# Kernel optimization log

Hardware: AMD Instinct MI355X
Metric: run time of the kernel (lower is better)

Reference implementation:

```python
import jax, jax.numpy as jnp
import numpy as np
from jax import lax

H = 1024       # hidden_size
I = 1024       # intermediate_size (per expert)
E = 16         # num_experts
TOP_K = 4      # num_active_experts


def setup_inputs() -> dict:
    key = jax.random.key(0)
    ks = jax.random.split(key, 9)
    std_gate = 0.02 / (E ** 0.5)
    return {
        "hidden_states": jax.random.normal(ks[0], (1, 2048, H), jnp.float32),
        "gate_w": jax.random.normal(ks[1], (E, H), jnp.float32) * std_gate,
        "expert_bias": jnp.zeros((E,), jnp.float32),
        "w1": jax.random.normal(ks[2], (E, I, H), jnp.float32) * 0.02,
        "w2": jax.random.normal(ks[3], (E, H, I), jnp.float32) * 0.02,
        "w3": jax.random.normal(ks[4], (E, I, H), jnp.float32) * 0.02,
        "sw1": jax.random.normal(ks[5], (I, H), jnp.float32) * 0.02,
        "sw2": jax.random.normal(ks[6], (H, I), jnp.float32) * 0.02,
        "sw3": jax.random.normal(ks[7], (I, H), jnp.float32) * 0.02,
    }


def _swiglu(x, wg, wd, wu):
    # Swish(x W1^T) * (x W3^T) then W2^T
    return (jax.nn.silu(x @ wg.T) * (x @ wu.T)) @ wd.T


def reference(hidden_states, gate_w, expert_bias, w1, w2, w3, sw1, sw2, sw3):
    B, S, Hd = hidden_states.shape
    x = hidden_states.reshape(-1, Hd)              # [T, H]
    T = x.shape[0]

    # ---- Router ----
    router_logits = x @ gate_w.T                   # [T, E]
    biased = router_logits + expert_bias           # loss-free balancing bias
    _, sel = lax.top_k(biased, TOP_K)              # [T, K] indices from biased logits
    raw = jnp.take_along_axis(router_logits, sel, axis=-1)  # weights from UNbiased logits
    rw = jax.nn.softmax(raw.astype(jnp.float32), axis=-1).astype(x.dtype)  # [T, K]

    # Dense combine weights g[t, e] = routing weight if e selected else 0
    g = jnp.zeros((T, E), x.dtype).at[jnp.arange(T)[:, None], sel].add(rw)

    # ---- Routed experts (mathematically equal to grouped dispatch) ----
    routed = jnp.zeros_like(x)
    for e in range(E):  # fixed small expert loop
        routed = routed + g[:, e:e + 1] * _swiglu(x, w1[e], w2[e], w3[e])

    # ---- Shared expert ----
    shared = _swiglu(x, sw1, sw2, sw3)

    out = (shared + routed).reshape(B, S, Hd)      # dropout p=0 -> identity
    return out
```

## Files before the change

kernel.cpp:

```cpp
#include <hip/hip_runtime.h>
#include <cstddef>
#include <cstdint>

#define T_TOK 2048
#define HD 1024
#define ID 1024
#define NE 16
#define TOPK 4
#define BM 128
#define BN 128
#define BK 32
#define MT_MAX 96
#define SLOT_CAP (MT_MAX * BM)

typedef float f32x4 __attribute__((ext_vector_type(4)));
typedef __bf16 bf16x8 __attribute__((ext_vector_type(8)));
typedef __bf16 bf16x4 __attribute__((ext_vector_type(4)));

#define WS_TILE_E 256
#define WS_LOGITS (256 + 8192 * 4 * 2 + 1024)
#define WS_SLOT_TOK (WS_LOGITS + T_TOK * NE * 4)
#define WS_SLOT_W (WS_SLOT_TOK + SLOT_CAP * 4)
#define WS_H1 (WS_SLOT_W + SLOT_CAP * 4)
#define WS_XB (WS_H1 + (size_t)SLOT_CAP * ID * 2)
#define WS_W1B (WS_XB + (size_t)T_TOK * HD * 2)
#define WS_W2B (WS_W1B + (size_t)NE * ID * HD * 2)
#define WS_W3B (WS_W2B + (size_t)NE * HD * ID * 2)
#define WS_SW1B (WS_W3B + (size_t)NE * ID * HD * 2)
#define WS_SW2B (WS_SW1B + (size_t)ID * HD * 2)
#define WS_SW3B (WS_SW2B + (size_t)HD * ID * 2)
#define WS_NEED (WS_SW3B + (size_t)ID * HD * 2)

__device__ __forceinline__ f32x4 mfma16(bf16x8 a, bf16x8 b, f32x4 c) {
  return __builtin_amdgcn_mfma_f32_16x16x32_bf16(a, b, c, 0, 0, 0);
}

__device__ __forceinline__ void st_bf16x4(__bf16* dst, float4 v) {
  __bf16 tmp[4] = {(__bf16)v.x, (__bf16)v.y, (__bf16)v.z, (__bf16)v.w};
  *(uint2*)dst = *(const uint2*)tmp;
}

__device__ __forceinline__ void gload16(const __bf16* g, __bf16* l) {
  __builtin_amdgcn_global_load_lds(
      (const __attribute__((address_space(1))) uint32_t*)g,
      (__attribute__((address_space(3))) uint32_t*)l, 16, 0, 0);
}

#define W4 ((size_t)1 << 22)
#define S4 ((size_t)1 << 18)
#define X4 ((size_t)1 << 19)
#define CVT4_TOTAL (3 * W4 + 3 * S4 + X4)
#define CVT_GRID 2048
#define LOGITS_BLOCKS (T_TOK / 4)

__global__ __launch_bounds__(256) void fused_pre(
    const float* __restrict__ w1, const float* __restrict__ w2,
    const float* __restrict__ w3, const float* __restrict__ sw1,
    const float* __restrict__ sw2, const float* __restrict__ sw3,
    const float* __restrict__ x, __bf16* __restrict__ w1b,
    __bf16* __restrict__ w2b, __bf16* __restrict__ w3b,
    __bf16* __restrict__ sw1b, __bf16* __restrict__ sw2b,
    __bf16* __restrict__ sw3b, __bf16* __restrict__ xb,
    const float* __restrict__ gw, float* __restrict__ logits) {
  int tid = threadIdx.x;
  if ((int)blockIdx.x < LOGITS_BLOCKS) {
    int wv = tid >> 6;
    int lane = tid & 63;
    int tok = blockIdx.x * 4 + wv;
    int e = lane >> 2;
    int q = lane & 3;
    const float4* xr = (const float4*)(x + (size_t)tok * HD) + q * 64;
    const float4* wr = (const float4*)(gw + (size_t)e * HD) + q * 64;
    float s0 = 0.f, s1 = 0.f;
#pragma unroll 8
    for (int i = 0; i < 64; i += 2) {
      float4 a0 = xr[i], w0 = wr[i];
      float4 a1 = xr[i + 1], w1v = wr[i + 1];
      s0 += a0.x * w0.x + a0.y * w0.y + a0.z * w0.z + a0.w * w0.w;
      s1 += a1.x * w1v.x + a1.y * w1v.y + a1.z * w1v.z + a1.w * w1v.w;
    }
    float s = s0 + s1;
    s += __shfl_xor(s, 1);
    s += __shfl_xor(s, 2);
    if (q == 0) logits[(size_t)tok * NE + e] = s;
    return;
  }
  size_t b = blockIdx.x - LOGITS_BLOCKS;
  const size_t stride = (size_t)CVT_GRID * 256;
  for (size_t i = b * 256 + tid; i < CVT4_TOTAL; i += stride) {
    const float* src;
    __bf16* dst;
    size_t off;
    if (i < 3 * W4) {
      size_t t = i >> 22;
      off = i & (W4 - 1);
      src = (t == 0) ? w1 : (t == 1) ? w2 : w3;
      dst = (t == 0) ? w1b : (t == 1) ? w2b : w3b;
    } else {
      size_t j = i - 3 * W4;
      if (j < 3 * S4) {
        size_t t = j >> 18;
        off = j & (S4 - 1);
        src = (t == 0) ? sw1 : (t == 1) ? sw2 : sw3;
        dst = (t == 0) ? sw1b : (t == 1) ? sw2b : sw3b;
      } else {
        off = j - 3 * S4;
        src = x;
        dst = xb;
      }
    }
    f32x4 v = __builtin_nontemporal_load((const f32x4*)src + off);
    bf16x4 o = {(__bf16)v[0], (__bf16)v[1], (__bf16)v[2], (__bf16)v[3]};
    *(bf16x4*)(dst + 4 * off) = o;
  }
}

__global__ __launch_bounds__(256) void router_logits(
    const float* __restrict__ x, const float* __restrict__ gw,
    float* __restrict__ logits) {
  int tid = threadIdx.x;
  int wv = tid >> 6;
  int lane = tid & 63;
  int tok = blockIdx.x * 4 + wv;
  int e = lane >> 2;
  int q = lane & 3;
  const float4* xr = (const float4*)(x + (size_t)tok * HD) + q * 64;
  const float4* wr = (const float4*)(gw + (size_t)e * HD) + q * 64;
  float s0 = 0.f, s1 = 0.f;
#pragma unroll 8
  for (int i = 0; i < 64; i += 2) {
    float4 a0 = xr[i], w0 = wr[i];
    float4 a1 = xr[i + 1], w1 = wr[i + 1];
    s0 += a0.x * w0.x + a0.y * w0.y + a0.z * w0.z + a0.w * w0.w;
    s1 += a1.x * w1.x + a1.y * w1.y + a1.z * w1.z + a1.w * w1.w;
  }
  float s = s0 + s1;
  s += __shfl_xor(s, 1);
  s += __shfl_xor(s, 2);
  if (q == 0) logits[(size_t)tok * NE + e] = s;
}

__global__ __launch_bounds__(256) void router_finish(
    const float* __restrict__ logits, const float* __restrict__ bias,
    int* __restrict__ tile_e, int* __restrict__ slot_tok,
    float* __restrict__ slot_w) {
  __shared__ int hist[NE];
  __shared__ int soff[NE + 1];
  __shared__ int fillp[NE];
  __shared__ unsigned lsel[T_TOK];
  __shared__ float4 lw4[T_TOK];

  int tid = threadIdx.x;
  if (tid < NE) { hist[tid] = 0; fillp[tid] = 0; }
  __syncthreads();

  float bb[NE];
#pragma unroll
  for (int e = 0; e < NE; ++e) bb[e] = bias[e];

  for (int j = 0; j < T_TOK / 256; ++j) {
    int t = tid + 256 * j;
    float lg[NE];
    const float4* lp = (const float4*)(logits + (size_t)t * NE);
#pragma unroll
    for (int q = 0; q < 4; ++q) {
      float4 v = lp[q];
      lg[4 * q] = v.x; lg[4 * q + 1] = v.y; lg[4 * q + 2] = v.z; lg[4 * q + 3] = v.w;
    }
    float b[NE];
#pragma unroll
    for (int e = 0; e < NE; ++e) b[e] = lg[e] + bb[e];

    int selk[TOPK];
    float raw[TOPK];
    unsigned used = 0;
#pragma unroll
    for (int k = 0; k < TOPK; ++k) {
      float best = -3.4e38f;
      int bi = 0;
#pragma unroll
      for (int e = 0; e < NE; ++e) {
        if (!((used >> e) & 1) && b[e] > best) { best = b[e]; bi = e; }
      }
      used |= (1u << bi);
      selk[k] = bi;
      raw[k] = lg[bi];
    }
    float m = raw[0];
#pragma unroll
    for (int k = 1; k < TOPK; ++k) m = fmaxf(m, raw[k]);
    float s = 0.f;
    float w[TOPK];
#pragma unroll
    for (int k = 0; k < TOPK; ++k) { w[k] = __expf(raw[k] - m); s += w[k]; }
    float inv = 1.f / s;
    lsel[t] = (unsigned)selk[0] | ((unsigned)selk[1] << 8) |
              ((unsigned)selk[2] << 16) | ((unsigned)selk[3] << 24);
    lw4[t] = make_float4(w[0] * inv, w[1] * inv, w[2] * inv, w[3] * inv);
#pragma unroll
    for (int k = 0; k < TOPK; ++k) atomicAdd(&hist[selk[k]], 1);
  }
  __syncthreads();

  if (tid == 0) {
    int o = 0;
    for (int e = 0; e < NE; ++e) { soff[e] = o; o += (hist[e] + BM - 1) & ~(BM - 1); }
    soff[NE] = o;
  }
  __syncthreads();
  int shared_base = soff[NE];
  int total = shared_base + T_TOK;
  for (int tt = tid; tt < MT_MAX; tt += 256) {
    int base = tt * BM;
    int ee = -1;
    if (base < shared_base) {
      ee = 0;
#pragma unroll
      for (int q = 1; q < NE; ++q) if (base >= soff[q]) ee = q;
    } else if (base < total) {
      ee = NE;
    }
    tile_e[tt] = ee;
  }

  for (int j = 0; j < T_TOK / 256; ++j) {
    int t = tid + 256 * j;
    unsigned ps = lsel[t];
    float4 wv = lw4[t];
    int e0 = ps & 255, e1 = (ps >> 8) & 255, e2 = (ps >> 16) & 255, e3 = ps >> 24;
    int p0 = atomicAdd(&fillp[e0], 1);
    slot_tok[soff[e0] + p0] = t; slot_w[soff[e0] + p0] = wv.x;
    int p1 = atomicAdd(&fillp[e1], 1);
    slot_tok[soff[e1] + p1] = t; slot_w[soff[e1] + p1] = wv.y;
    int p2 = atomicAdd(&fillp[e2], 1);
    slot_tok[soff[e2] + p2] = t; slot_w[soff[e2] + p2] = wv.z;
    int p3 = atomicAdd(&fillp[e3], 1);
    slot_tok[soff[e3] + p3] = t; slot_w[soff[e3] + p3] = wv.w;
  }

  for (int s = tid; s < shared_base; s += 256) {
    int e = 0;
#pragma unroll
    for (int q = 1; q < NE; ++q) if (s >= soff[q]) e = q;
    if (s >= soff[e] + hist[e]) { slot_tok[s] = -1; slot_w[s] = 0.f; }
  }
  for (int s = shared_base + tid; s < total; s += 256) {
    slot_tok[s] = s - shared_base;
    slot_w[s] = 1.0f;
  }
}


__global__ __launch_bounds__(256, 2) void pass1_bf16(
    const __bf16* __restrict__ xb, const int* __restrict__ slot_tok,
    const int* __restrict__ tile_e, const __bf16* __restrict__ w1b,
    const __bf16* __restrict__ w3b, const __bf16* __restrict__ sw1b,
    const __bf16* __restrict__ sw3b, __bf16* __restrict__ h1) {
  int mt = blockIdx.y;
  int e = tile_e[mt];
  if (e < 0) return;
  int n0 = blockIdx.x * BN;
  int m0 = mt * BM;

  const __bf16* wg = (e == NE) ? sw1b : w1b + (size_t)e * ID * HD;
  const __bf16* wu = (e == NE) ? sw3b : w3b + (size_t)e * ID * HD;

  __shared__ __align__(16) __bf16 As[2][BM * BK];
  __shared__ __align__(16) __bf16 Bg[2][BN * BK];
  __shared__ __align__(16) __bf16 Bu[2][BN * BK];

  int tid = threadIdx.x;
  int r0 = tid >> 2, r1 = r0 + 64;
  int c8 = ((tid & 3) ^ ((r0 >> 1) & 3)) * 8;
  int tok0 = slot_tok[m0 + r0]; if (tok0 < 0) tok0 = 0;
  int tok1 = slot_tok[m0 + r1]; if (tok1 < 0) tok1 = 0;
  const __bf16* gA0 = xb + (size_t)tok0 * HD + c8;
  const __bf16* gA1 = xb + (size_t)tok1 * HD + c8;
  const __bf16* gG0 = wg + (size_t)(n0 + r0) * HD + c8;
  const __bf16* gG1 = wg + (size_t)(n0 + r1) * HD + c8;
  const __bf16* gU0 = wu + (size_t)(n0 + r0) * HD + c8;
  const __bf16* gU1 = wu + (size_t)(n0 + r1) * HD + c8;

  int wave = tid >> 6, lane = tid & 63;
  int wm = (wave >> 1) * 64, wn = (wave & 1) * 64;
  int l16 = lane & 15, kch = lane >> 4;
  int kk8 = (kch ^ ((l16 >> 1) & 3)) * 8;

  f32x4 accg[4][4] = {};
  f32x4 accu[4][4] = {};

  auto stage = [&](int B, int k0) {
    gload16(gA0 + k0, &As[B][(size_t)tid * 8]);
    gload16(gA1 + k0, &As[B][(size_t)(tid + 256) * 8]);
    gload16(gG0 + k0, &Bg[B][(size_t)tid * 8]);
    gload16(gG1 + k0, &Bg[B][(size_t)(tid + 256) * 8]);
    gload16(gU0 + k0, &Bu[B][(size_t)tid * 8]);
    gload16(gU1 + k0, &Bu[B][(size_t)(tid + 256) * 8]);
  };
  auto body = [&](int B) {
    bf16x8 af[4], gf[4], uf[4];
#pragma unroll
    for (int i = 0; i < 4; ++i) {
      af[i] = *(const bf16x8*)(&As[B][(wm + i * 16 + l16) * BK + kk8]);
      gf[i] = *(const bf16x8*)(&Bg[B][(wn + i * 16 + l16) * BK + kk8]);
      uf[i] = *(const bf16x8*)(&Bu[B][(wn + i * 16 + l16) * BK + kk8]);
    }
    asm volatile("s_waitcnt lgkmcnt(0)" ::: "memory");
    __builtin_amdgcn_s_barrier();
    __builtin_amdgcn_sched_barrier(0);
#pragma unroll
    for (int mi = 0; mi < 4; ++mi)
#pragma unroll
      for (int ni = 0; ni < 4; ++ni) {
        accg[mi][ni] = mfma16(af[mi], gf[ni], accg[mi][ni]);
        accu[mi][ni] = mfma16(af[mi], uf[ni], accu[mi][ni]);
      }
  };

  stage(0, 0);
#pragma unroll 1
  for (int k = 0; k < HD / BK - 1; ++k) {
    int cur = k & 1;
    stage(cur ^ 1, (k + 1) * BK);
    asm volatile("s_waitcnt vmcnt(6)" ::: "memory");
    __builtin_amdgcn_s_barrier();
    __builtin_amdgcn_sched_barrier(0);
    body(cur);
  }
  asm volatile("s_waitcnt vmcnt(0)" ::: "memory");
  __builtin_amdgcn_s_barrier();
  __builtin_amdgcn_sched_barrier(0);
  body((HD / BK - 1) & 1);

#pragma unroll
  for (int mi = 0; mi < 4; ++mi) {
#pragma unroll
    for (int ni = 0; ni < 4; ++ni) {
#pragma unroll
      for (int j = 0; j < 4; ++j) {
        int row = m0 + wm + mi * 16 + kch * 4 + j;
        int col = n0 + wn + ni * 16 + l16;
        float g = accg[mi][ni][j];
        float u = accu[mi][ni][j];
        float hv = (g / (1.f + __expf(-g))) * u;
        h1[(size_t)row * ID + col] = (__bf16)hv;
      }
    }
  }
}

__global__ __launch_bounds__(256, 3) void pass2_bf16(
    const __bf16* __restrict__ h1, const int* __restrict__ slot_tok,
    const float* __restrict__ slot_w, const int* __restrict__ tile_e,
    const __bf16* __restrict__ w2b, const __bf16* __restrict__ sw2b,
    float* __restrict__ out) {
  int mt = blockIdx.y;
  int e = tile_e[mt];
  if (e < 0) return;
  int n0 = blockIdx.x * BN;
  int m0 = mt * BM;

  const __bf16* wd = (e == NE) ? sw2b : w2b + (size_t)e * HD * ID;

  __shared__ __align__(16) __bf16 As[2][BM * BK];
  __shared__ __align__(16) __bf16 Bs[2][BN * BK];

  int tid = threadIdx.x;
  int r0 = tid >> 2, r1 = r0 + 64;
  int c8 = ((tid & 3) ^ ((r0 >> 1) & 3)) * 8;
  const __bf16* gA0 = h1 + (size_t)(m0 + r0) * ID + c8;
  const __bf16* gA1 = h1 + (size_t)(m0 + r1) * ID + c8;
  const __bf16* gB0 = wd + (size_t)(n0 + r0) * ID + c8;
  const __bf16* gB1 = wd + (size_t)(n0 + r1) * ID + c8;

  int wave = tid >> 6, lane = tid & 63;
  int wm = (wave >> 1) * 64, wn = (wave & 1) * 64;
  int l16 = lane & 15, kch = lane >> 4;
  int kk8 = (kch ^ ((l16 >> 1) & 3)) * 8;

  f32x4 acc[4][4] = {};

  auto stage = [&](int B, int k0) {
    gload16(gA0 + k0, &As[B][(size_t)tid * 8]);
    gload16(gA1 + k0, &As[B][(size_t)(tid + 256) * 8]);
    gload16(gB0 + k0, &Bs[B][(size_t)tid * 8]);
    gload16(gB1 + k0, &Bs[B][(size_t)(tid + 256) * 8]);
  };
  auto body = [&](int B) {
    bf16x8 af[4], bf[4];
#pragma unroll
    for (int i = 0; i < 4; ++i) {
      af[i] = *(const bf16x8*)(&As[B][(wm + i * 16 + l16) * BK + kk8]);
      bf[i] = *(const bf16x8*)(&Bs[B][(wn + i * 16 + l16) * BK + kk8]);
    }
    asm volatile("s_waitcnt lgkmcnt(0)" ::: "memory");
    __builtin_amdgcn_s_barrier();
    __builtin_amdgcn_sched_barrier(0);
#pragma unroll
    for (int mi = 0; mi < 4; ++mi)
#pragma unroll
      for (int ni = 0; ni < 4; ++ni)
        acc[mi][ni] = mfma16(af[mi], bf[ni], acc[mi][ni]);
  };

  stage(0, 0);
#pragma unroll 1
  for (int k = 0; k < ID / BK - 1; ++k) {
    int cur = k & 1;
    stage(cur ^ 1, (k + 1) * BK);
    asm volatile("s_waitcnt vmcnt(4)" ::: "memory");
    __builtin_amdgcn_s_barrier();
    __builtin_amdgcn_sched_barrier(0);
    body(cur);
  }
  asm volatile("s_waitcnt vmcnt(0)" ::: "memory");
  __builtin_amdgcn_s_barrier();
  __builtin_amdgcn_sched_barrier(0);
  body((ID / BK - 1) & 1);

#pragma unroll
  for (int mi = 0; mi < 4; ++mi) {
#pragma unroll
    for (int j = 0; j < 4; ++j) {
      int row = m0 + wm + mi * 16 + kch * 4 + j;
      int token = slot_tok[row];
      if (token < 0) continue;
      float wgt = slot_w[row];
#pragma unroll
      for (int ni = 0; ni < 4; ++ni) {
        int col = n0 + wn + ni * 16 + l16;
        atomicAdd(out + (size_t)token * HD + col, wgt * acc[mi][ni][j]);
      }
    }
  }
}


__global__ __launch_bounds__(256, 2) void pass1_gemm(
    const float* __restrict__ x, const int* __restrict__ slot_tok,
    const int* __restrict__ tile_e, const float* __restrict__ w1,
    const float* __restrict__ w3, const float* __restrict__ sw1,
    const float* __restrict__ sw3, __bf16* __restrict__ h1) {
  int mt = blockIdx.x;
  int e = tile_e[mt];
  if (e < 0) return;
  int n0 = blockIdx.y * BN;
  int m0 = mt * BM;

  const float* wg;
  const float* wu;
  if (e == NE) { wg = sw1; wu = sw3; }
  else { wg = w1 + (size_t)e * ID * HD; wu = w3 + (size_t)e * ID * HD; }

  __shared__ __bf16 As[BM][BK + 8];
  __shared__ __bf16 Bg[BN][BK + 8];
  __shared__ __bf16 Bu[BN][BK + 8];

  int tid = threadIdx.x;
  int lrow = tid >> 1;
  int lcol = (tid & 1) * 16;
  int tokenA = slot_tok[m0 + lrow];
  const float* aptr = x + (size_t)(tokenA < 0 ? 0 : tokenA) * HD + lcol;
  const float* gptr = wg + (size_t)(n0 + lrow) * HD + lcol;
  const float* uptr = wu + (size_t)(n0 + lrow) * HD + lcol;

  int wave = tid >> 6, lane = tid & 63;
  int wm = (wave >> 1) * 64, wn = (wave & 1) * 64;
  int l16 = lane & 15, kch = lane >> 4;

  f32x4 accg[4][4] = {};
  f32x4 accu[4][4] = {};

  for (int k0 = 0; k0 < HD; k0 += BK) {
    float4 av[4], gv[4], uv[4];
#pragma unroll
    for (int j = 0; j < 4; ++j) {
      av[j] = (tokenA >= 0) ? *(const float4*)(aptr + k0 + 4 * j)
                            : make_float4(0.f, 0.f, 0.f, 0.f);
      gv[j] = *(const float4*)(gptr + k0 + 4 * j);
      uv[j] = *(const float4*)(uptr + k0 + 4 * j);
    }
    __syncthreads();
#pragma unroll
    for (int j = 0; j < 4; ++j) {
      st_bf16x4(&As[lrow][lcol + 4 * j], av[j]);
      st_bf16x4(&Bg[lrow][lcol + 4 * j], gv[j]);
      st_bf16x4(&Bu[lrow][lcol + 4 * j], uv[j]);
    }
    __syncthreads();

    bf16x8 af[4], gf[4], uf[4];
#pragma unroll
    for (int i = 0; i < 4; ++i) {
      af[i] = *(const bf16x8*)(&As[wm + i * 16 + l16][kch * 8]);
      gf[i] = *(const bf16x8*)(&Bg[wn + i * 16 + l16][kch * 8]);
      uf[i] = *(const bf16x8*)(&Bu[wn + i * 16 + l16][kch * 8]);
    }
#pragma unroll
    for (int mi = 0; mi < 4; ++mi)
#pragma unroll
      for (int ni = 0; ni < 4; ++ni) {
        accg[mi][ni] = mfma16(af[mi], gf[ni], accg[mi][ni]);
        accu[mi][ni] = mfma16(af[mi], uf[ni], accu[mi][ni]);
      }
  }

#pragma unroll
  for (int mi = 0; mi < 4; ++mi) {
#pragma unroll
    for (int ni = 0; ni < 4; ++ni) {
#pragma unroll
      for (int j = 0; j < 4; ++j) {
        int row = m0 + wm + mi * 16 + kch * 4 + j;
        int col = n0 + wn + ni * 16 + l16;
        float g = accg[mi][ni][j];
        float u = accu[mi][ni][j];
        float hv = (g / (1.f + __expf(-g))) * u;
        h1[(size_t)row * ID + col] = (__bf16)hv;
      }
    }
  }
}

__global__ __launch_bounds__(256, 2) void pass2_gemm(
    const __bf16* __restrict__ h1, const int* __restrict__ slot_tok,
    const float* __restrict__ slot_w, const int* __restrict__ tile_e,
    const float* __restrict__ w2, const float* __restrict__ sw2,
    float* __restrict__ out) {
  int mt = blockIdx.x;
  int e = tile_e[mt];
  if (e < 0) return;
  int n0 = blockIdx.y * BN;
  int m0 = mt * BM;

  const float* wd = (e == NE) ? sw2 : (w2 + (size_t)e * HD * ID);

  __shared__ __bf16 As[BM][BK + 8];
  __shared__ __bf16 Bs[BN][BK + 8];

  int tid = threadIdx.x;
  int lrow = tid >> 1;
  int lcol = (tid & 1) * 16;
  const __bf16* aptr = h1 + (size_t)(m0 + lrow) * ID + lcol;
  const float* bptr = wd + (size_t)(n0 + lrow) * ID + lcol;

  int wave = tid >> 6, lane = tid & 63;
  int wm = (wave >> 1) * 64, wn = (wave & 1) * 64;
  int l16 = lane & 15, kch = lane >> 4;

  f32x4 acc[4][4] = {};

  for (int k0 = 0; k0 < ID; k0 += BK) {
    uint4 a0 = *(const uint4*)(aptr + k0);
    uint4 a1 = *(const uint4*)(aptr + k0 + 8);
    float4 bv[4];
#pragma unroll
    for (int j = 0; j < 4; ++j) bv[j] = *(const float4*)(bptr + k0 + 4 * j);
    __syncthreads();
    *(uint4*)(&As[lrow][lcol]) = a0;
    *(uint4*)(&As[lrow][lcol + 8]) = a1;
#pragma unroll
    for (int j = 0; j < 4; ++j) st_bf16x4(&Bs[lrow][lcol + 4 * j], bv[j]);
    __syncthreads();

    bf16x8 af[4], bf[4];
#pragma unroll
    for (int i = 0; i < 4; ++i) {
      af[i] = *(const bf16x8*)(&As[wm + i * 16 + l16][kch * 8]);
      bf[i] = *(const bf16x8*)(&Bs[wn + i * 16 + l16][kch * 8]);
    }
#pragma unroll
    for (int mi = 0; mi < 4; ++mi)
#pragma unroll
      for (int ni = 0; ni < 4; ++ni)
        acc[mi][ni] = mfma16(af[mi], bf[ni], acc[mi][ni]);
  }

#pragma unroll
  for (int mi = 0; mi < 4; ++mi) {
#pragma unroll
    for (int j = 0; j < 4; ++j) {
      int row = m0 + wm + mi * 16 + kch * 4 + j;
      int token = slot_tok[row];
      if (token < 0) continue;
      float wgt = slot_w[row];
#pragma unroll
      for (int ni = 0; ni < 4; ++ni) {
        int col = n0 + wn + ni * 16 + l16;
        atomicAdd(out + (size_t)token * HD + col, wgt * acc[mi][ni][j]);
      }
    }
  }
}

extern "C" void kernel_launch(void* const* d_in, const int* in_sizes, int n_in,
                              void* d_out, int out_size, void* d_ws, size_t ws_size,
                              hipStream_t stream) {
  const float* x = (const float*)d_in[0];
  const float* gate_w = (const float*)d_in[1];
  const float* ebias = (const float*)d_in[2];
  const float* w1 = (const float*)d_in[3];
  const float* w2 = (const float*)d_in[4];
  const float* w3 = (const float*)d_in[5];
  const float* sw1 = (const float*)d_in[6];
  const float* sw2 = (const float*)d_in[7];
  const float* sw3 = (const float*)d_in[8];
  float* out = (float*)d_out;

  char* ws = (char*)d_ws;
  int* tile_e = (int*)(ws + WS_TILE_E);
  float* logits = (float*)(ws + WS_LOGITS);
  int* slot_tok = (int*)(ws + WS_SLOT_TOK);
  float* slot_w = (float*)(ws + WS_SLOT_W);
  __bf16* h1 = (__bf16*)(ws + WS_H1);

  hipMemsetAsync(d_out, 0, (size_t)T_TOK * HD * sizeof(float), stream);

  if (ws_size >= WS_NEED) {
    __bf16* xb = (__bf16*)(ws + WS_XB);
    __bf16* w1b = (__bf16*)(ws + WS_W1B);
    __bf16* w2b = (__bf16*)(ws + WS_W2B);
    __bf16* w3b = (__bf16*)(ws + WS_W3B);
    __bf16* sw1b = (__bf16*)(ws + WS_SW1B);
    __bf16* sw2b = (__bf16*)(ws + WS_SW2B);
    __bf16* sw3b = (__bf16*)(ws + WS_SW3B);

    fused_pre<<<LOGITS_BLOCKS + CVT_GRID, 256, 0, stream>>>(
        w1, w2, w3, sw1, sw2, sw3, x, w1b, w2b, w3b, sw1b, sw2b, sw3b, xb,
        gate_w, logits);
    router_finish<<<1, 256, 0, stream>>>(logits, ebias, tile_e, slot_tok, slot_w);

    pass1_bf16<<<dim3(ID / BN, MT_MAX), 256, 0, stream>>>(
        xb, slot_tok, tile_e, w1b, w3b, sw1b, sw3b, h1);
    pass2_bf16<<<dim3(HD / BN, MT_MAX), 256, 0, stream>>>(
        h1, slot_tok, slot_w, tile_e, w2b, sw2b, out);
  } else {
    router_logits<<<T_TOK / 4, 256, 0, stream>>>(x, gate_w, logits);
    router_finish<<<1, 256, 0, stream>>>(logits, ebias, tile_e, slot_tok, slot_w);
    pass1_gemm<<<dim3(MT_MAX, ID / BN), 256, 0, stream>>>(x, slot_tok, tile_e, w1,
                                                          w3, sw1, sw3, h1);
    pass2_gemm<<<dim3(MT_MAX, HD / BN), 256, 0, stream>>>(h1, slot_tok, slot_w,
                                                          tile_e, w2, sw2, out);
  }
}
```

Baseline: 256.6 us.

## Convert w1/w3 to bf16 inside pass1 instead of a separate pre-pass

The pre-pass no longer converts the w1, w3, sw1 and sw3 weights to bf16. It now converts only w2, sw2 and x, using 8-wide vector stores. pass1 reads the fp32 gate and up weights directly, converts them in registers and writes them into double-buffered swizzled LDS. The activation tile still arrives through direct global-to-LDS loads. This drops one full fp32 read plus bf16 write and reread of about 64 MB of weights. The cost is that each weight tile is reread in fp32 once per m-tile, and pass1 now waits on vmcnt(0) synchronously. The fallback fp32 kernels and the workspace size check are removed.

```diff
diff --git a/kernel.cpp b/kernel.cpp
--- a/kernel.cpp
+++ b/kernel.cpp
@@ -10,34 +10,32 @@
 #define BM 128
 #define BN 128
 #define BK 32
+#define NK1 (HD / BK)
 #define MT_MAX 96
 #define SLOT_CAP (MT_MAX * BM)
 
 typedef float f32x4 __attribute__((ext_vector_type(4)));
 typedef __bf16 bf16x8 __attribute__((ext_vector_type(8)));
-typedef __bf16 bf16x4 __attribute__((ext_vector_type(4)));
 
 #define WS_TILE_E 256
-#define WS_LOGITS (256 + 8192 * 4 * 2 + 1024)
+#define WS_LOGITS 4096
 #define WS_SLOT_TOK (WS_LOGITS + T_TOK * NE * 4)
 #define WS_SLOT_W (WS_SLOT_TOK + SLOT_CAP * 4)
 #define WS_H1 (WS_SLOT_W + SLOT_CAP * 4)
 #define WS_XB (WS_H1 + (size_t)SLOT_CAP * ID * 2)
-#define WS_W1B (WS_XB + (size_t)T_TOK * HD * 2)
-#define WS_W2B (WS_W1B + (size_t)NE * ID * HD * 2)
-#define WS_W3B (WS_W2B + (size_t)NE * HD * ID * 2)
-#define WS_SW1B (WS_W3B + (size_t)NE * ID * HD * 2)
-#define WS_SW2B (WS_SW1B + (size_t)ID * HD * 2)
-#define WS_SW3B (WS_SW2B + (size_t)HD * ID * 2)
-#define WS_NEED (WS_SW3B + (size_t)ID * HD * 2)
+#define WS_W2B (WS_XB + (size_t)T_TOK * HD * 2)
+#define WS_SW2B (WS_W2B + (size_t)NE * HD * ID * 2)
+#define WS_NEED (WS_SW2B + (size_t)ID * HD * 2)
 
 __device__ __forceinline__ f32x4 mfma16(bf16x8 a, bf16x8 b, f32x4 c) {
   return __builtin_amdgcn_mfma_f32_16x16x32_bf16(a, b, c, 0, 0, 0);
 }
 
-__device__ __forceinline__ void st_bf16x4(__bf16* dst, float4 v) {
-  __bf16 tmp[4] = {(__bf16)v.x, (__bf16)v.y, (__bf16)v.z, (__bf16)v.w};
-  *(uint2*)dst = *(const uint2*)tmp;
+__device__ __forceinline__ bf16x8 pack8(float4 a, float4 b) {
+  bf16x8 o;
+  o[0] = (__bf16)a.x; o[1] = (__bf16)a.y; o[2] = (__bf16)a.z; o[3] = (__bf16)a.w;
+  o[4] = (__bf16)b.x; o[5] = (__bf16)b.y; o[6] = (__bf16)b.z; o[7] = (__bf16)b.w;
+  return o;
 }
 
 __device__ __forceinline__ void gload16(const __bf16* g, __bf16* l) {
@@ -46,21 +44,17 @@
       (__attribute__((address_space(3))) uint32_t*)l, 16, 0, 0);
 }
 
-#define W4 ((size_t)1 << 22)
-#define S4 ((size_t)1 << 18)
-#define X4 ((size_t)1 << 19)
-#define CVT4_TOTAL (3 * W4 + 3 * S4 + X4)
-#define CVT_GRID 2048
+#define W2G ((size_t)NE * HD * ID / 8)
+#define SWG ((size_t)ID * HD / 8)
+#define XG ((size_t)T_TOK * HD / 8)
+#define CVT_TOT (W2G + SWG + XG)
+#define CVTB 1536
 #define LOGITS_BLOCKS (T_TOK / 4)
 
 __global__ __launch_bounds__(256) void fused_pre(
-    const float* __restrict__ w1, const float* __restrict__ w2,
-    const float* __restrict__ w3, const float* __restrict__ sw1,
-    const float* __restrict__ sw2, const float* __restrict__ sw3,
-    const float* __restrict__ x, __bf16* __restrict__ w1b,
-    __bf16* __restrict__ w2b, __bf16* __restrict__ w3b,
-    __bf16* __restrict__ sw1b, __bf16* __restrict__ sw2b,
-    __bf16* __restrict__ sw3b, __bf16* __restrict__ xb,
+    const float* __restrict__ w2, const float* __restrict__ sw2,
+    const float* __restrict__ x, __bf16* __restrict__ w2b,
+    __bf16* __restrict__ sw2b, __bf16* __restrict__ xb,
     const float* __restrict__ gw, float* __restrict__ logits) {
   int tid = threadIdx.x;
   if ((int)blockIdx.x < LOGITS_BLOCKS) {
@@ -86,58 +80,18 @@
     return;
   }
   size_t b = blockIdx.x - LOGITS_BLOCKS;
-  const size_t stride = (size_t)CVT_GRID * 256;
-  for (size_t i = b * 256 + tid; i < CVT4_TOTAL; i += stride) {
+  const size_t stride = (size_t)CVTB * 256;
+  for (size_t i = b * 256 + tid; i < CVT_TOT; i += stride) {
     const float* src;
     __bf16* dst;
     size_t off;
-    if (i < 3 * W4) {
-      size_t t = i >> 22;
-      off = i & (W4 - 1);
-      src = (t == 0) ? w1 : (t == 1) ? w2 : w3;
-      dst = (t == 0) ? w1b : (t == 1) ? w2b : w3b;
-    } else {
-      size_t j = i - 3 * W4;
-      if (j < 3 * S4) {
-        size_t t = j >> 18;
-        off = j & (S4 - 1);
-        src = (t == 0) ? sw1 : (t == 1) ? sw2 : sw3;
-        dst = (t == 0) ? sw1b : (t == 1) ? sw2b : sw3b;
-      } else {
-        off = j - 3 * S4;
-        src = x;
-        dst = xb;
-      }
-    }
-    f32x4 v = __builtin_nontemporal_load((const f32x4*)src + off);
-    bf16x4 o = {(__bf16)v[0], (__bf16)v[1], (__bf16)v[2], (__bf16)v[3]};
-    *(bf16x4*)(dst + 4 * off) = o;
-  }
-}
-
-__global__ __launch_bounds__(256) void router_logits(
-    const float* __restrict__ x, const float* __restrict__ gw,
-    float* __restrict__ logits) {
-  int tid = threadIdx.x;
-  int wv = tid >> 6;
-  int lane = tid & 63;
-  int tok = blockIdx.x * 4 + wv;
-  int e = lane >> 2;
-  int q = lane & 3;
-  const float4* xr = (const float4*)(x + (size_t)tok * HD) + q * 64;
-  const float4* wr = (const float4*)(gw + (size_t)e * HD) + q * 64;
-  float s0 = 0.f, s1 = 0.f;
-#pragma unroll 8
-  for (int i = 0; i < 64; i += 2) {
-    float4 a0 = xr[i], w0 = wr[i];
-    float4 a1 = xr[i + 1], w1 = wr[i + 1];
-    s0 += a0.x * w0.x + a0.y * w0.y + a0.z * w0.z + a0.w * w0.w;
-    s1 += a1.x * w1.x + a1.y * w1.y + a1.z * w1.z + a1.w * w1.w;
-  }
-  float s = s0 + s1;
-  s += __shfl_xor(s, 1);
-  s += __shfl_xor(s, 2);
-  if (q == 0) logits[(size_t)tok * NE + e] = s;
+    if (i < W2G) { src = w2; dst = w2b; off = i; }
+    else if (i < W2G + SWG) { src = sw2; dst = sw2b; off = i - W2G; }
+    else { src = x; dst = xb; off = i - W2G - SWG; }
+    const float4* p = (const float4*)src + 2 * off;
+    float4 a = p[0], c = p[1];
+    *(bf16x8*)(dst + 8 * off) = pack8(a, c);
+  }
 }
 
 __global__ __launch_bounds__(256) void router_finish(
@@ -250,20 +204,19 @@
   }
 }
 
-
 __global__ __launch_bounds__(256, 2) void pass1_bf16(
     const __bf16* __restrict__ xb, const int* __restrict__ slot_tok,
-    const int* __restrict__ tile_e, const __bf16* __restrict__ w1b,
-    const __bf16* __restrict__ w3b, const __bf16* __restrict__ sw1b,
-    const __bf16* __restrict__ sw3b, __bf16* __restrict__ h1) {
+    const int* __restrict__ tile_e, const float* __restrict__ w1,
+    const float* __restrict__ w3, const float* __restrict__ sw1,
+    const float* __restrict__ sw3, __bf16* __restrict__ h1) {
   int mt = blockIdx.y;
   int e = tile_e[mt];
   if (e < 0) return;
   int n0 = blockIdx.x * BN;
   int m0 = mt * BM;
 
-  const __bf16* wg = (e == NE) ? sw1b : w1b + (size_t)e * ID * HD;
-  const __bf16* wu = (e == NE) ? sw3b : w3b + (size_t)e * ID * HD;
+  const float* wg = (e == NE) ? sw1 : w1 + (size_t)e * ID * HD;
+  const float* wu = (e == NE) ? sw3 : w3 + (size_t)e * ID * HD;
 
   __shared__ __align__(16) __bf16 As[2][BM * BK];
   __shared__ __align__(16) __bf16 Bg[2][BN * BK];
@@ -276,10 +229,14 @@
   int tok1 = slot_tok[m0 + r1]; if (tok1 < 0) tok1 = 0;
   const __bf16* gA0 = xb + (size_t)tok0 * HD + c8;
   const __bf16* gA1 = xb + (size_t)tok1 * HD + c8;
-  const __bf16* gG0 = wg + (size_t)(n0 + r0) * HD + c8;
-  const __bf16* gG1 = wg + (size_t)(n0 + r1) * HD + c8;
-  const __bf16* gU0 = wu + (size_t)(n0 + r0) * HD + c8;
-  const __bf16* gU1 = wu + (size_t)(n0 + r1) * HD + c8;
+
+  int brow = tid >> 1;
+  int bhalf = tid & 1;
+  int bsw = (brow >> 1) & 3;
+  const float* gW = wg + (size_t)(n0 + brow) * HD + bhalf * 16;
+  const float* gU = wu + (size_t)(n0 + brow) * HD + bhalf * 16;
+  int slot0 = (((bhalf * 2) ^ bsw) * 8) + brow * BK;
+  int slot1 = (((bhalf * 2 + 1) ^ bsw) * 8) + brow * BK;
 
   int wave = tid >> 6, lane = tid & 63;
   int wm = (wave >> 1) * 64, wn = (wave & 1) * 64;
@@ -289,24 +246,53 @@
   f32x4 accg[4][4] = {};
   f32x4 accu[4][4] = {};
 
-  auto stage = [&](int B, int k0) {
-    gload16(gA0 + k0, &As[B][(size_t)tid * 8]);
-    gload16(gA1 + k0, &As[B][(size_t)(tid + 256) * 8]);
-    gload16(gG0 + k0, &Bg[B][(size_t)tid * 8]);
-    gload16(gG1 + k0, &Bg[B][(size_t)(tid + 256) * 8]);
-    gload16(gU0 + k0, &Bu[B][(size_t)tid * 8]);
-    gload16(gU1 + k0, &Bu[B][(size_t)(tid + 256) * 8]);
-  };
-  auto body = [&](int B) {
-    bf16x8 af[4], gf[4], uf[4];
-#pragma unroll
-    for (int i = 0; i < 4; ++i) {
-      af[i] = *(const bf16x8*)(&As[B][(wm + i * 16 + l16) * BK + kk8]);
-      gf[i] = *(const bf16x8*)(&Bg[B][(wn + i * 16 + l16) * BK + kk8]);
-      uf[i] = *(const bf16x8*)(&Bu[B][(wn + i * 16 + l16) * BK + kk8]);
-    }
+  {
+    float4 g0 = *(const float4*)(gW);
+    float4 g1 = *(const float4*)(gW + 4);
+    float4 g2 = *(const float4*)(gW + 8);
+    float4 g3 = *(const float4*)(gW + 12);
+    float4 v0 = *(const float4*)(gU);
+    float4 v1 = *(const float4*)(gU + 4);
+    float4 v2 = *(const float4*)(gU + 8);
+    float4 v3 = *(const float4*)(gU + 12);
+    gload16(gA0, &As[0][(size_t)tid * 8]);
+    gload16(gA1, &As[0][(size_t)(tid + 256) * 8]);
+    asm volatile("s_waitcnt vmcnt(0)" ::: "memory");
+    *(bf16x8*)(&Bg[0][slot0]) = pack8(g0, g1);
+    *(bf16x8*)(&Bg[0][slot1]) = pack8(g2, g3);
+    *(bf16x8*)(&Bu[0][slot0]) = pack8(v0, v1);
+    *(bf16x8*)(&Bu[0][slot1]) = pack8(v2, v3);
     asm volatile("s_waitcnt lgkmcnt(0)" ::: "memory");
     __builtin_amdgcn_s_barrier();
+  }
+
+#pragma unroll 1
+  for (int k = 0; k < NK1; ++k) {
+    int cur = k & 1;
+    bool pf = (k + 1 < NK1);
+    float4 g0, g1, g2, g3, v0, v1, v2, v3;
+    if (pf) {
+      const float* pW = gW + (k + 1) * BK;
+      const float* pU = gU + (k + 1) * BK;
+      g0 = *(const float4*)(pW);
+      g1 = *(const float4*)(pW + 4);
+      g2 = *(const float4*)(pW + 8);
+      g3 = *(const float4*)(pW + 12);
+      v0 = *(const float4*)(pU);
+      v1 = *(const float4*)(pU + 4);
+      v2 = *(const float4*)(pU + 8);
+      v3 = *(const float4*)(pU + 12);
+      gload16(gA0 + (k + 1) * BK, &As[cur ^ 1][(size_t)tid * 8]);
+      gload16(gA1 + (k + 1) * BK, &As[cur ^ 1][(size_t)(tid + 256) * 8]);
+    }
+    bf16x8 af[4], gf[4], uf[4];
+#pragma unroll
+    for (int i = 0; i < 4; ++i) {
+      af[i] = *(const bf16x8*)(&As[cur][(wm + i * 16 + l16) * BK + kk8]);
+      gf[i] = *(const bf16x8*)(&Bg[cur][(wn + i * 16 + l16) * BK + kk8]);
+      uf[i] = *(const bf16x8*)(&Bu[cur][(wn + i * 16 + l16) * BK + kk8]);
+    }
+    asm volatile("s_waitcnt lgkmcnt(0)" ::: "memory");
     __builtin_amdgcn_sched_barrier(0);
 #pragma unroll
     for (int mi = 0; mi < 4; ++mi)
@@ -315,22 +301,16 @@
         accg[mi][ni] = mfma16(af[mi], gf[ni], accg[mi][ni]);
         accu[mi][ni] = mfma16(af[mi], uf[ni], accu[mi][ni]);
       }
-  };
-
-  stage(0, 0);
-#pragma unroll 1
-  for (int k = 0; k < HD / BK - 1; ++k) {
-    int cur = k & 1;
-    stage(cur ^ 1, (k + 1) * BK);
-    asm volatile("s_waitcnt vmcnt(6)" ::: "memory");
-    __builtin_amdgcn_s_barrier();
-    __builtin_amdgcn_sched_barrier(0);
-    body(cur);
-  }
-  asm volatile("s_waitcnt vmcnt(0)" ::: "memory");
-  __builtin_amdgcn_s_barrier();
-  __builtin_amdgcn_sched_barrier(0);
-  body((HD / BK - 1) & 1);
+    if (pf) {
+      asm volatile("s_waitcnt vmcnt(0)" ::: "memory");
+      *(bf16x8*)(&Bg[cur ^ 1][slot0]) = pack8(g0, g1);
+      *(bf16x8*)(&Bg[cur ^ 1][slot1]) = pack8(g2, g3);
+      *(bf16x8*)(&Bu[cur ^ 1][slot0]) = pack8(v0, v1);
+      *(bf16x8*)(&Bu[cur ^ 1][slot1]) = pack8(v2, v3);
+      asm volatile("s_waitcnt lgkmcnt(0)" ::: "memory");
+      __builtin_amdgcn_s_barrier();
+    }
+  }
 
 #pragma unroll
   for (int mi = 0; mi < 4; ++mi) {
@@ -417,164 +397,6 @@
   __builtin_amdgcn_s_barrier();
   __builtin_amdgcn_sched_barrier(0);
   body((ID / BK - 1) & 1);
-
-#pragma unroll
-  for (int mi = 0; mi < 4; ++mi) {
-#pragma unroll
-    for (int j = 0; j < 4; ++j) {
-      int row = m0 + wm + mi * 16 + kch * 4 + j;
-      int token = slot_tok[row];
-      if (token < 0) continue;
-      float wgt = slot_w[row];
-#pragma unroll
-      for (int ni = 0; ni < 4; ++ni) {
-        int col = n0 + wn + ni * 16 + l16;
-        atomicAdd(out + (size_t)token * HD + col, wgt * acc[mi][ni][j]);
-      }
-    }
-  }
-}
-
-
-__global__ __launch_bounds__(256, 2) void pass1_gemm(
-    const float* __restrict__ x, const int* __restrict__ slot_tok,
-    const int* __restrict__ tile_e, const float* __restrict__ w1,
-    const float* __restrict__ w3, const float* __restrict__ sw1,
-    const float* __restrict__ sw3, __bf16* __restrict__ h1) {
-  int mt = blockIdx.x;
-  int e = tile_e[mt];
-  if (e < 0) return;
-  int n0 = blockIdx.y * BN;
-  int m0 = mt * BM;
-
-  const float* wg;
-  const float* wu;
-  if (e == NE) { wg = sw1; wu = sw3; }
-  else { wg = w1 + (size_t)e * ID * HD; wu = w3 + (size_t)e * ID * HD; }
-
-  __shared__ __bf16 As[BM][BK + 8];
-  __shared__ __bf16 Bg[BN][BK + 8];
-  __shared__ __bf16 Bu[BN][BK + 8];
-
-  int tid = threadIdx.x;
-  int lrow = tid >> 1;
-  int lcol = (tid & 1) * 16;
-  int tokenA = slot_tok[m0 + lrow];
-  const float* aptr = x + (size_t)(tokenA < 0 ? 0 : tokenA) * HD + lcol;
-  const float* gptr = wg + (size_t)(n0 + lrow) * HD + lcol;
-  const float* uptr = wu + (size_t)(n0 + lrow) * HD + lcol;
-
-  int wave = tid >> 6, lane = tid & 63;
-  int wm = (wave >> 1) * 64, wn = (wave & 1) * 64;
-  int l16 = lane & 15, kch = lane >> 4;
-
-  f32x4 accg[4][4] = {};
-  f32x4 accu[4][4] = {};
-
-  for (int k0 = 0; k0 < HD; k0 += BK) {
-    float4 av[4], gv[4], uv[4];
-#pragma unroll
-    for (int j = 0; j < 4; ++j) {
-      av[j] = (tokenA >= 0) ? *(const float4*)(aptr + k0 + 4 * j)
-                            : make_float4(0.f, 0.f, 0.f, 0.f);
-      gv[j] = *(const float4*)(gptr + k0 + 4 * j);
-      uv[j] = *(const float4*)(uptr + k0 + 4 * j);
-    }
-    __syncthreads();
-#pragma unroll
-    for (int j = 0; j < 4; ++j) {
-      st_bf16x4(&As[lrow][lcol + 4 * j], av[j]);
-      st_bf16x4(&Bg[lrow][lcol + 4 * j], gv[j]);
-      st_bf16x4(&Bu[lrow][lcol + 4 * j], uv[j]);
-    }
-    __syncthreads();
-
-    bf16x8 af[4], gf[4], uf[4];
-#pragma unroll
-    for (int i = 0; i < 4; ++i) {
-      af[i] = *(const bf16x8*)(&As[wm + i * 16 + l16][kch * 8]);
-      gf[i] = *(const bf16x8*)(&Bg[wn + i * 16 + l16][kch * 8]);
-      uf[i] = *(const bf16x8*)(&Bu[wn + i * 16 + l16][kch * 8]);
-    }
-#pragma unroll
-    for (int mi = 0; mi < 4; ++mi)
-#pragma unroll
-      for (int ni = 0; ni < 4; ++ni) {
-        accg[mi][ni] = mfma16(af[mi], gf[ni], accg[mi][ni]);
-        accu[mi][ni] = mfma16(af[mi], uf[ni], accu[mi][ni]);
-      }
-  }
-
-#pragma unroll
-  for (int mi = 0; mi < 4; ++mi) {
-#pragma unroll
-    for (int ni = 0; ni < 4; ++ni) {
-#pragma unroll
-      for (int j = 0; j < 4; ++j) {
-        int row = m0 + wm + mi * 16 + kch * 4 + j;
-        int col = n0 + wn + ni * 16 + l16;
-        float g = accg[mi][ni][j];
-        float u = accu[mi][ni][j];
-        float hv = (g / (1.f + __expf(-g))) * u;
-        h1[(size_t)row * ID + col] = (__bf16)hv;
-      }
-    }
-  }
-}
-
-__global__ __launch_bounds__(256, 2) void pass2_gemm(
-    const __bf16* __restrict__ h1, const int* __restrict__ slot_tok,
-    const float* __restrict__ slot_w, const int* __restrict__ tile_e,
-    const float* __restrict__ w2, const float* __restrict__ sw2,
-    float* __restrict__ out) {
-  int mt = blockIdx.x;
-  int e = tile_e[mt];
-  if (e < 0) return;
-  int n0 = blockIdx.y * BN;
-  int m0 = mt * BM;
-
-  const float* wd = (e == NE) ? sw2 : (w2 + (size_t)e * HD * ID);
-
-  __shared__ __bf16 As[BM][BK + 8];
-  __shared__ __bf16 Bs[BN][BK + 8];
-
-  int tid = threadIdx.x;
-  int lrow = tid >> 1;
-  int lcol = (tid & 1) * 16;
-  const __bf16* aptr = h1 + (size_t)(m0 + lrow) * ID + lcol;
-  const float* bptr = wd + (size_t)(n0 + lrow) * ID + lcol;
-
-  int wave = tid >> 6, lane = tid & 63;
-  int wm = (wave >> 1) * 64, wn = (wave & 1) * 64;
-  int l16 = lane & 15, kch = lane >> 4;
-
-  f32x4 acc[4][4] = {};
-
-  for (int k0 = 0; k0 < ID; k0 += BK) {
-    uint4 a0 = *(const uint4*)(aptr + k0);
-    uint4 a1 = *(const uint4*)(aptr + k0 + 8);
-    float4 bv[4];
-#pragma unroll
-    for (int j = 0; j < 4; ++j) bv[j] = *(const float4*)(bptr + k0 + 4 * j);
-    __syncthreads();
-    *(uint4*)(&As[lrow][lcol]) = a0;
-    *(uint4*)(&As[lrow][lcol + 8]) = a1;
-#pragma unroll
-    for (int j = 0; j < 4; ++j) st_bf16x4(&Bs[lrow][lcol + 4 * j], bv[j]);
-    __syncthreads();
-
-    bf16x8 af[4], bf[4];
-#pragma unroll
-    for (int i = 0; i < 4; ++i) {
-      af[i] = *(const bf16x8*)(&As[wm + i * 16 + l16][kch * 8]);
-      bf[i] = *(const bf16x8*)(&Bs[wn + i * 16 + l16][kch * 8]);
-    }
-#pragma unroll
-    for (int mi = 0; mi < 4; ++mi)
-#pragma unroll
-      for (int ni = 0; ni < 4; ++ni)
-        acc[mi][ni] = mfma16(af[mi], bf[ni], acc[mi][ni]);
-  }
 
 #pragma unroll
   for (int mi = 0; mi < 4; ++mi) {
@@ -613,33 +435,18 @@
   int* slot_tok = (int*)(ws + WS_SLOT_TOK);
   float* slot_w = (float*)(ws + WS_SLOT_W);
   __bf16* h1 = (__bf16*)(ws + WS_H1);
+  __bf16* xb = (__bf16*)(ws + WS_XB);
+  __bf16* w2b = (__bf16*)(ws + WS_W2B);
+  __bf16* sw2b = (__bf16*)(ws + WS_SW2B);
 
   hipMemsetAsync(d_out, 0, (size_t)T_TOK * HD * sizeof(float), stream);
 
-  if (ws_size >= WS_NEED) {
-    __bf16* xb = (__bf16*)(ws + WS_XB);
-    __bf16* w1b = (__bf16*)(ws + WS_W1B);
-    __bf16* w2b = (__bf16*)(ws + WS_W2B);
-    __bf16* w3b = (__bf16*)(ws + WS_W3B);
-    __bf16* sw1b = (__bf16*)(ws + WS_SW1B);
-    __bf16* sw2b = (__bf16*)(ws + WS_SW2B);
-    __bf16* sw3b = (__bf16*)(ws + WS_SW3B);
-
-    fused_pre<<<LOGITS_BLOCKS + CVT_GRID, 256, 0, stream>>>(
-        w1, w2, w3, sw1, sw2, sw3, x, w1b, w2b, w3b, sw1b, sw2b, sw3b, xb,
-        gate_w, logits);
-    router_finish<<<1, 256, 0, stream>>>(logits, ebias, tile_e, slot_tok, slot_w);
-
-    pass1_bf16<<<dim3(ID / BN, MT_MAX), 256, 0, stream>>>(
-        xb, slot_tok, tile_e, w1b, w3b, sw1b, sw3b, h1);
-    pass2_bf16<<<dim3(HD / BN, MT_MAX), 256, 0, stream>>>(
-        h1, slot_tok, slot_w, tile_e, w2b, sw2b, out);
-  } else {
-    router_logits<<<T_TOK / 4, 256, 0, stream>>>(x, gate_w, logits);
-    router_finish<<<1, 256, 0, stream>>>(logits, ebias, tile_e, slot_tok, slot_w);
-    pass1_gemm<<<dim3(MT_MAX, ID / BN), 256, 0, stream>>>(x, slot_tok, tile_e, w1,
-                                                          w3, sw1, sw3, h1);
-    pass2_gemm<<<dim3(MT_MAX, HD / BN), 256, 0, stream>>>(h1, slot_tok, slot_w,
-                                                          tile_e, w2, sw2, out);
-  }
-}
+  fused_pre<<<LOGITS_BLOCKS + CVTB, 256, 0, stream>>>(w2, sw2, x, w2b, sw2b, xb,
+                                                      gate_w, logits);
+  router_finish<<<1, 256, 0, stream>>>(logits, ebias, tile_e, slot_tok, slot_w);
+
+  pass1_bf16<<<dim3(ID / BN, MT_MAX), 256, 0, stream>>>(
+      xb, slot_tok, tile_e, w1, w3, sw1, sw3, h1);
+  pass2_bf16<<<dim3(HD / BN, MT_MAX), 256, 0, stream>>>(
+      h1, slot_tok, slot_w, tile_e, w2b, sw2b, out);
+}
```

New measurement: 287.7 us. +12.1%, slower.
